# Kernel optimization log

Hardware: AMD Instinct MI355X
Metric: run time of the kernel (lower is better)

## Reference

```python
import jax, jax.numpy as jnp
import numpy as np

N, C_IN, H, W = 32, 16, 256, 256
C_OUT, K = 64, 3

def setup_inputs() -> dict:
    key = jax.random.key(0)
    kx, kw, kb = jax.random.split(key, 3)
    x = jax.random.normal(kx, (N, C_IN, H, W), dtype=jnp.float32)
    # PyTorch Conv2d default init: U(-b, b), b = 1/sqrt(fan_in)
    bound = 1.0 / np.sqrt(C_IN * K * K)
    conv_weight = jax.random.uniform(kw, (C_OUT, C_IN, K, K), minval=-bound, maxval=bound, dtype=jnp.float32)
    conv_bias = jax.random.uniform(kb, (C_OUT,), minval=-bound, maxval=bound, dtype=jnp.float32)
    return {"x": x, "conv_weight": conv_weight, "conv_bias": conv_bias}

def reference(x, conv_weight, conv_bias):
    # conv2d, stride=1, padding=0 (VALID), NCHW / OIHW
    y = jax.lax.conv_general_dilated(
        x, conv_weight,
        window_strides=(1, 1), padding="VALID",
        dimension_numbers=("NCHW", "OIHW", "NCHW"))
    y = y + conv_bias[None, :, None, None]
    # min over output channels (keepdim -> 1 channel), then double tanh
    y = jnp.min(y, axis=1, keepdims=True)  # [N,1,OH,OW]
    return jnp.tanh(jnp.tanh(y))
```

## Files before the change

### kernel.cpp

```cpp
#include <hip/hip_runtime.h>

typedef __bf16 bf16x8 __attribute__((ext_vector_type(8)));
typedef unsigned short us8 __attribute__((ext_vector_type(8)));
typedef unsigned short us2 __attribute__((ext_vector_type(2)));
typedef float f32x16 __attribute__((ext_vector_type(16)));

#define N_IMG 32
#define CI 16
#define HH 256
#define WW 256
#define CO 64
#define OHH 254
#define OWW 254
#define RPB 2
#define NBLK_H (OHH / RPB)
#define NBLK (N_IMG * NBLK_H)

#define XS_W 258
#define XS_C 24
#define WP_SHORTS (CO * 160)
#define WS_NEEDED ((size_t)WP_SHORTS * 2)

__device__ __forceinline__ unsigned short f2bf(float f) {
  union { float f; unsigned u; } v; v.f = f;
  return (unsigned short)((v.u + 0x7FFFu + ((v.u >> 16) & 1u)) >> 16);
}

#if defined(__has_builtin)
#if __has_builtin(__builtin_amdgcn_cvt_pk_bf16_f32)
#define HAVE_CVT_PK 1
#endif
#endif

__device__ __forceinline__ us2 cvt2(float a, float b) {
#ifdef HAVE_CVT_PK
  typedef __bf16 bf16x2 __attribute__((ext_vector_type(2)));
  bf16x2 r = __builtin_amdgcn_cvt_pk_bf16_f32(a, b);
  return __builtin_bit_cast(us2, r);
#else
  us2 r; r[0] = f2bf(a); r[1] = f2bf(b); return r;
#endif
}

__device__ __forceinline__ float fast_tanh(float x) {
  float cx = fminf(fmaxf(x, -15.f), 15.f);
  float e = __expf(2.f * cx);
  return (e - 1.f) / (e + 1.f);
}

__global__ void prep_w(const float* __restrict__ wg, const float* __restrict__ bg,
                       unsigned short* __restrict__ wp) {
  int idx = blockIdx.x * 256 + threadIdx.x;
  if (idx >= WP_SHORTS) return;
  int oc = idx / 160;
  int k = idx - oc * 160;
  int tap = k >> 4, ci = k & 15;
  float v;
  if (tap < 9)      v = wg[oc * 144 + ci * 9 + tap];
  else if (ci == 0) v = bg[oc];
  else              v = 0.f;
  wp[idx] = f2bf(v);
}

__global__ __launch_bounds__(256, 3)
void conv_fused(const float* __restrict__ xg, const unsigned short* __restrict__ wp,
                float* __restrict__ out) {
  __shared__ __align__(16) unsigned short xs[(RPB + 2) * XS_W * XS_C];
  const int t = threadIdx.x;
  const int n = blockIdx.x / NBLK_H;
  const int oh0 = (blockIdx.x - n * NBLK_H) * RPB;

  {
    const float* src = xg + (size_t)n * (CI * HH * WW) + t;
    float v[RPB + 2][16];
#pragma unroll
    for (int r = 0; r < RPB + 2; ++r)
#pragma unroll
      for (int j = 0; j < 16; ++j)
        v[r][j] = src[((size_t)j * HH + (oh0 + r)) * WW];
#pragma unroll
    for (int r = 0; r < RPB + 2; ++r) {
      union { us8 v8[2]; us2 v2[8]; } pk;
#pragma unroll
      for (int j = 0; j < 8; ++j) pk.v2[j] = cvt2(v[r][2 * j], v[r][2 * j + 1]);
      *(us8*)(xs + (r * XS_W + t) * XS_C) = pk.v8[0];
      *(us8*)(xs + (r * XS_W + t) * XS_C + 8) = pk.v8[1];
    }
  }
  if (t < 32 * (RPB + 2)) {
    int r = t >> 5, rem = t & 31;
    int w = 256 + (rem >> 4), ci = rem & 15;
    xs[(r * XS_W + w) * XS_C + ci] = 0;
  }
  __syncthreads();

  const int lane = t & 63, wave = t >> 6;
  const int lr = lane & 31, qh = lane >> 5;

  const unsigned short* wpl = wp + lr * 160 + qh * 8;
  bf16x8 afrag[2][10];
#pragma unroll
  for (int mt = 0; mt < 2; ++mt)
#pragma unroll
    for (int tap = 0; tap < 10; ++tap)
      afrag[mt][tap] =
          __builtin_bit_cast(bf16x8, *(const us8*)(wpl + mt * 32 * 160 + tap * 16));

  us8 onev = {};
  if (qh == 0) onev[0] = 0x3F80;
  const bf16x8 xone = __builtin_bit_cast(bf16x8, onev);

  const int pb = wave * 64;

#pragma unroll
  for (int r = 0; r < RPB; ++r) {
    f32x16 acc[2][2];
#pragma unroll
    for (int a = 0; a < 2; ++a)
#pragma unroll
      for (int b = 0; b < 2; ++b)
#pragma unroll
        for (int e = 0; e < 16; ++e) acc[a][b][e] = 0.f;

#pragma unroll
    for (int tap = 0; tap < 9; ++tap) {
      const int kh = tap / 3, kw = tap - kh * 3;
#pragma unroll
      for (int nt = 0; nt < 2; ++nt) {
        bf16x8 xf = __builtin_bit_cast(
            bf16x8,
            *(const us8*)(xs + ((r + kh) * XS_W + pb + nt * 32 + lr + kw) * XS_C +
                          qh * 8));
        acc[0][nt] = __builtin_amdgcn_mfma_f32_32x32x16_bf16(afrag[0][tap], xf,
                                                             acc[0][nt], 0, 0, 0);
        acc[1][nt] = __builtin_amdgcn_mfma_f32_32x32x16_bf16(afrag[1][tap], xf,
                                                             acc[1][nt], 0, 0, 0);
      }
    }
#pragma unroll
    for (int nt = 0; nt < 2; ++nt) {
      acc[0][nt] = __builtin_amdgcn_mfma_f32_32x32x16_bf16(afrag[0][9], xone,
                                                           acc[0][nt], 0, 0, 0);
      acc[1][nt] = __builtin_amdgcn_mfma_f32_32x32x16_bf16(afrag[1][9], xone,
                                                           acc[1][nt], 0, 0, 0);
    }

    float vmin[2];
#pragma unroll
    for (int nt = 0; nt < 2; ++nt) {
      float v = acc[0][nt][0];
#pragma unroll
      for (int e = 1; e < 16; ++e) v = fminf(v, acc[0][nt][e]);
#pragma unroll
      for (int e = 0; e < 16; ++e) v = fminf(v, acc[1][nt][e]);
      v = fminf(v, __shfl_xor(v, 32, 64));
      vmin[nt] = fast_tanh(fast_tanh(v));
    }
    float res = (lane < 32) ? vmin[0] : vmin[1];
    int ow = pb + lane;
    if (ow < OWW) out[((size_t)n * OHH + (oh0 + r)) * OWW + ow] = res;
  }
}

#define WS_K 168
__global__ __launch_bounds__(256, 2)
void conv_min_tanh(const float* __restrict__ xg, const float* __restrict__ wg,
                   const float* __restrict__ bg, float* __restrict__ out) {
  __shared__ __align__(16) unsigned short xs[3 * XS_W * XS_C];
  __shared__ __align__(16) unsigned short ws[CO * WS_K];
  const int t = threadIdx.x;
  const int n = blockIdx.x / OHH;
  const int oh = blockIdx.x % OHH;
#pragma unroll
  for (int i = 0; i < 36; ++i) {
    int f = i * 256 + t;
    int oc = f / 144;
    int r = f - oc * 144;
    int ci = r / 9;
    int tap = r - ci * 9;
    ws[oc * WS_K + tap * 16 + ci] = f2bf(wg[f]);
  }
  if (t < CO) ws[t * WS_K + 144] = f2bf(bg[t]);
  for (int i = t; i < CO * 15; i += 256) {
    int oc = i / 15;
    ws[oc * WS_K + 145 + (i - oc * 15)] = 0;
  }
  {
    const size_t base_n = (size_t)n * CI * HH * WW;
#pragma unroll
    for (int kh = 0; kh < 3; ++kh) {
#pragma unroll
      for (int half = 0; half < 2; ++half) {
        float v[8];
#pragma unroll
        for (int j = 0; j < 8; ++j) {
          int ci = half * 8 + j;
          v[j] = xg[base_n + ((size_t)ci * HH + (oh + kh)) * WW + t];
        }
        us8 pk;
#pragma unroll
        for (int j = 0; j < 8; ++j) pk[j] = f2bf(v[j]);
        *(us8*)(xs + (kh * XS_W + t) * XS_C + half * 8) = pk;
      }
    }
  }
  if (t < 96) {
    int kh = t >> 5;
    int rem = t & 31;
    int w = 256 + (rem >> 4);
    int ci = rem & 15;
    xs[(kh * XS_W + w) * XS_C + ci] = 0;
  }
  __syncthreads();
  const int lane = t & 63, wave = t >> 6;
  const int lr = lane & 31, qh = lane >> 5;
  bf16x8 afrag[2][10];
#pragma unroll
  for (int mt = 0; mt < 2; ++mt) {
    const unsigned short* wq = ws + (mt * 32 + lr) * WS_K + qh * 8;
#pragma unroll
    for (int tap = 0; tap < 10; ++tap)
      afrag[mt][tap] = __builtin_bit_cast(bf16x8, *(const us8*)(wq + tap * 16));
  }
  f32x16 acc[2][2];
#pragma unroll
  for (int a = 0; a < 2; ++a)
#pragma unroll
    for (int b = 0; b < 2; ++b)
#pragma unroll
      for (int e = 0; e < 16; ++e) acc[a][b][e] = 0.f;
  const unsigned short* xq = xs + (wave * 64 + lr) * XS_C + qh * 8;
#pragma unroll
  for (int tap = 0; tap < 9; ++tap) {
    const int kh = tap / 3, kw = tap - kh * 3;
#pragma unroll
    for (int nt = 0; nt < 2; ++nt) {
      bf16x8 xf = __builtin_bit_cast(
          bf16x8, *(const us8*)(xq + (kh * XS_W + nt * 32 + kw) * XS_C));
      acc[0][nt] = __builtin_amdgcn_mfma_f32_32x32x16_bf16(afrag[0][tap], xf,
                                                           acc[0][nt], 0, 0, 0);
      acc[1][nt] = __builtin_amdgcn_mfma_f32_32x32x16_bf16(afrag[1][tap], xf,
                                                           acc[1][nt], 0, 0, 0);
    }
  }
  {
    us8 one = {};
    if (qh == 0) one[0] = 0x3F80;
    bf16x8 xone = __builtin_bit_cast(bf16x8, one);
#pragma unroll
    for (int nt = 0; nt < 2; ++nt) {
      acc[0][nt] = __builtin_amdgcn_mfma_f32_32x32x16_bf16(afrag[0][9], xone,
                                                           acc[0][nt], 0, 0, 0);
      acc[1][nt] = __builtin_amdgcn_mfma_f32_32x32x16_bf16(afrag[1][9], xone,
                                                           acc[1][nt], 0, 0, 0);
    }
  }
  float vmin[2];
#pragma unroll
  for (int nt = 0; nt < 2; ++nt) {
    float v = acc[0][nt][0];
#pragma unroll
    for (int e = 1; e < 16; ++e) v = fminf(v, acc[0][nt][e]);
#pragma unroll
    for (int e = 0; e < 16; ++e) v = fminf(v, acc[1][nt][e]);
    v = fminf(v, __shfl_xor(v, 32, 64));
    vmin[nt] = fast_tanh(fast_tanh(v));
  }
  float res = (lane < 32) ? vmin[0] : vmin[1];
  int ow = wave * 64 + lane;
  if (ow < OWW) out[((size_t)n * OHH + oh) * OWW + ow] = res;
}

extern "C" void kernel_launch(void* const* d_in, const int* in_sizes, int n_in,
                              void* d_out, int out_size, void* d_ws, size_t ws_size,
                              hipStream_t stream) {
  const float* x = (const float*)d_in[0];
  const float* w = (const float*)d_in[1];
  const float* b = (const float*)d_in[2];
  float* out = (float*)d_out;
  if (ws_size >= WS_NEEDED) {
    unsigned short* wp = (unsigned short*)d_ws;
    prep_w<<<dim3((WP_SHORTS + 255) / 256), dim3(256), 0, stream>>>(w, b, wp);
    conv_fused<<<dim3(NBLK), dim3(256), 0, stream>>>(x, wp, out);
  } else {
    conv_min_tanh<<<dim3(N_IMG * OHH), dim3(256), 0, stream>>>(x, w, b, out);
  }
}
```

Baseline: 213.3 us.

## Pipeline row tiles through a shared-memory ring buffer in persistent span blocks

Each block now processes a 16-row span of one image instead of 2 rows. Input rows go into a 6-slot circular shared-memory buffer, so halo rows are reused across tiles rather than reloaded. Loads for the next two rows are issued before the MFMA work on the current tile, which overlaps global memory latency with compute. The cost is fewer blocks (512) at lower occupancy (launch bounds 2) and a barrier per tile.

```diff
diff --git a/kernel.cpp b/kernel.cpp
--- a/kernel.cpp
+++ b/kernel.cpp
@@ -13,8 +13,8 @@
 #define OHH 254
 #define OWW 254
 #define RPB 2
-#define NBLK_H (OHH / RPB)
-#define NBLK (N_IMG * NBLK_H)
+#define SLOTS 6
+#define SPANS 16
 
 #define XS_W 258
 #define XS_C 24
@@ -62,37 +62,40 @@
   wp[idx] = f2bf(v);
 }
 
-__global__ __launch_bounds__(256, 3)
-void conv_fused(const float* __restrict__ xg, const unsigned short* __restrict__ wp,
-                float* __restrict__ out) {
-  __shared__ __align__(16) unsigned short xs[(RPB + 2) * XS_W * XS_C];
+__global__ __launch_bounds__(256, 2)
+void conv_pipe(const float* __restrict__ xg, const unsigned short* __restrict__ wp,
+               float* __restrict__ out) {
+  __shared__ __align__(16) unsigned short xs[SLOTS * XS_W * XS_C];
   const int t = threadIdx.x;
-  const int n = blockIdx.x / NBLK_H;
-  const int oh0 = (blockIdx.x - n * NBLK_H) * RPB;
-
+  const int n = blockIdx.x >> 4;
+  const int sp = blockIdx.x & 15;
+  const int ntiles = (sp == SPANS - 1) ? 7 : 8;
+  int oh0 = sp * 16;
+
+  const float* src = xg + (size_t)n * (CI * HH * WW) + t;
+
+  if (t < 32 * SLOTS) {
+    int sl = t >> 5, rem = t & 31;
+    int w = 256 + (rem >> 4), ci = rem & 15;
+    xs[(sl * XS_W + w) * XS_C + ci] = 0;
+  }
   {
-    const float* src = xg + (size_t)n * (CI * HH * WW) + t;
-    float v[RPB + 2][16];
-#pragma unroll
-    for (int r = 0; r < RPB + 2; ++r)
+    float v[4][16];
+#pragma unroll
+    for (int r = 0; r < 4; ++r)
 #pragma unroll
       for (int j = 0; j < 16; ++j)
         v[r][j] = src[((size_t)j * HH + (oh0 + r)) * WW];
 #pragma unroll
-    for (int r = 0; r < RPB + 2; ++r) {
+    for (int r = 0; r < 4; ++r) {
       union { us8 v8[2]; us2 v2[8]; } pk;
 #pragma unroll
       for (int j = 0; j < 8; ++j) pk.v2[j] = cvt2(v[r][2 * j], v[r][2 * j + 1]);
-      *(us8*)(xs + (r * XS_W + t) * XS_C) = pk.v8[0];
-      *(us8*)(xs + (r * XS_W + t) * XS_C + 8) = pk.v8[1];
-    }
-  }
-  if (t < 32 * (RPB + 2)) {
-    int r = t >> 5, rem = t & 31;
-    int w = 256 + (rem >> 4), ci = rem & 15;
-    xs[(r * XS_W + w) * XS_C + ci] = 0;
-  }
-  __syncthreads();
+      const int sl = (oh0 + r) % SLOTS;
+      *(us8*)(xs + (sl * XS_W + t) * XS_C) = pk.v8[0];
+      *(us8*)(xs + (sl * XS_W + t) * XS_C + 8) = pk.v8[1];
+    }
+  }
 
   const int lane = t & 63, wave = t >> 6;
   const int lr = lane & 31, qh = lane >> 5;
@@ -110,55 +113,88 @@
   if (qh == 0) onev[0] = 0x3F80;
   const bf16x8 xone = __builtin_bit_cast(bf16x8, onev);
 
-  const int pb = wave * 64;
-
-#pragma unroll
-  for (int r = 0; r < RPB; ++r) {
-    f32x16 acc[2][2];
-#pragma unroll
-    for (int a = 0; a < 2; ++a)
-#pragma unroll
-      for (int b = 0; b < 2; ++b)
-#pragma unroll
-        for (int e = 0; e < 16; ++e) acc[a][b][e] = 0.f;
-
-#pragma unroll
-    for (int tap = 0; tap < 9; ++tap) {
-      const int kh = tap / 3, kw = tap - kh * 3;
+  const int pbl = wave * 64 + lr;
+  __syncthreads();
+
+  int m6 = oh0 % SLOTS;
+  for (int tt = 0; tt < ntiles; ++tt) {
+    const bool more = (tt + 1 < ntiles);
+
+    float v[2][16];
+    if (more) {
+#pragma unroll
+      for (int rr = 0; rr < 2; ++rr)
+#pragma unroll
+        for (int j = 0; j < 16; ++j)
+          v[rr][j] = src[((size_t)j * HH + (oh0 + 4 + rr)) * WW];
+    }
+
+#pragma unroll
+    for (int r = 0; r < RPB; ++r) {
+      f32x16 acc[2][2];
+#pragma unroll
+      for (int a = 0; a < 2; ++a)
+#pragma unroll
+        for (int b = 0; b < 2; ++b)
+#pragma unroll
+          for (int e = 0; e < 16; ++e) acc[a][b][e] = 0.f;
+
+#pragma unroll
+      for (int tap = 0; tap < 9; ++tap) {
+        const int kh = tap / 3, kw = tap - kh * 3;
+        int sl = m6 + r + kh;
+        if (sl >= SLOTS) sl -= SLOTS;
+#pragma unroll
+        for (int nt = 0; nt < 2; ++nt) {
+          bf16x8 xf = __builtin_bit_cast(
+              bf16x8,
+              *(const us8*)(xs + (sl * XS_W + pbl + nt * 32 + kw) * XS_C + qh * 8));
+          acc[0][nt] = __builtin_amdgcn_mfma_f32_32x32x16_bf16(afrag[0][tap], xf,
+                                                               acc[0][nt], 0, 0, 0);
+          acc[1][nt] = __builtin_amdgcn_mfma_f32_32x32x16_bf16(afrag[1][tap], xf,
+                                                               acc[1][nt], 0, 0, 0);
+        }
+      }
 #pragma unroll
       for (int nt = 0; nt < 2; ++nt) {
-        bf16x8 xf = __builtin_bit_cast(
-            bf16x8,
-            *(const us8*)(xs + ((r + kh) * XS_W + pb + nt * 32 + lr + kw) * XS_C +
-                          qh * 8));
-        acc[0][nt] = __builtin_amdgcn_mfma_f32_32x32x16_bf16(afrag[0][tap], xf,
+        acc[0][nt] = __builtin_amdgcn_mfma_f32_32x32x16_bf16(afrag[0][9], xone,
                                                              acc[0][nt], 0, 0, 0);
-        acc[1][nt] = __builtin_amdgcn_mfma_f32_32x32x16_bf16(afrag[1][tap], xf,
+        acc[1][nt] = __builtin_amdgcn_mfma_f32_32x32x16_bf16(afrag[1][9], xone,
                                                              acc[1][nt], 0, 0, 0);
       }
-    }
-#pragma unroll
-    for (int nt = 0; nt < 2; ++nt) {
-      acc[0][nt] = __builtin_amdgcn_mfma_f32_32x32x16_bf16(afrag[0][9], xone,
-                                                           acc[0][nt], 0, 0, 0);
-      acc[1][nt] = __builtin_amdgcn_mfma_f32_32x32x16_bf16(afrag[1][9], xone,
-                                                           acc[1][nt], 0, 0, 0);
-    }
-
-    float vmin[2];
-#pragma unroll
-    for (int nt = 0; nt < 2; ++nt) {
-      float v = acc[0][nt][0];
-#pragma unroll
-      for (int e = 1; e < 16; ++e) v = fminf(v, acc[0][nt][e]);
-#pragma unroll
-      for (int e = 0; e < 16; ++e) v = fminf(v, acc[1][nt][e]);
-      v = fminf(v, __shfl_xor(v, 32, 64));
-      vmin[nt] = fast_tanh(fast_tanh(v));
-    }
-    float res = (lane < 32) ? vmin[0] : vmin[1];
-    int ow = pb + lane;
-    if (ow < OWW) out[((size_t)n * OHH + (oh0 + r)) * OWW + ow] = res;
+
+      float vmin[2];
+#pragma unroll
+      for (int nt = 0; nt < 2; ++nt) {
+        float vm = acc[0][nt][0];
+#pragma unroll
+        for (int e = 1; e < 16; ++e) vm = fminf(vm, acc[0][nt][e]);
+#pragma unroll
+        for (int e = 0; e < 16; ++e) vm = fminf(vm, acc[1][nt][e]);
+        vm = fminf(vm, __shfl_xor(vm, 32, 64));
+        vmin[nt] = fast_tanh(fast_tanh(vm));
+      }
+      float res = (lane < 32) ? vmin[0] : vmin[1];
+      int ow = wave * 64 + lane;
+      if (ow < OWW) out[((size_t)n * OHH + (oh0 + r)) * OWW + ow] = res;
+    }
+
+    if (more) {
+#pragma unroll
+      for (int rr = 0; rr < 2; ++rr) {
+        union { us8 v8[2]; us2 v2[8]; } pk;
+#pragma unroll
+        for (int j = 0; j < 8; ++j) pk.v2[j] = cvt2(v[rr][2 * j], v[rr][2 * j + 1]);
+        int sl = m6 + 4 + rr;
+        if (sl >= SLOTS) sl -= SLOTS;
+        *(us8*)(xs + (sl * XS_W + t) * XS_C) = pk.v8[0];
+        *(us8*)(xs + (sl * XS_W + t) * XS_C + 8) = pk.v8[1];
+      }
+    }
+    __syncthreads();
+    oh0 += 2;
+    m6 += 2;
+    if (m6 >= SLOTS) m6 -= SLOTS;
   }
 }
 
@@ -281,7 +317,7 @@
   if (ws_size >= WS_NEEDED) {
     unsigned short* wp = (unsigned short*)d_ws;
     prep_w<<<dim3((WP_SHORTS + 255) / 256), dim3(256), 0, stream>>>(w, b, wp);
-    conv_fused<<<dim3(NBLK), dim3(256), 0, stream>>>(x, wp, out);
+    conv_pipe<<<dim3(N_IMG * SPANS), dim3(256), 0, stream>>>(x, wp, out);
   } else {
     conv_min_tanh<<<dim3(N_IMG * OHH), dim3(256), 0, stream>>>(x, w, b, out);
   }
```

After: 215.4 us. No clear change (+1.0%).
